# Optimization experiments

Measured on AMD Instinct MI355X. Metric: run time of the kernel, lower is better.

The kernel has to match this reference:

```python
import jax, jax.numpy as jnp
import numpy as np

B, S, D, H = 4, 2048, 512, 8
DH = D // H


def setup_inputs() -> dict:
    key = jax.random.key(0)
    ks = jax.random.split(key, 7)
    scale = 1.0 / np.sqrt(DH)  # mimic nn.Linear init magnitude
    return {
        "x": jax.random.normal(ks[0], (B, S, D), dtype=jnp.float32),
        "Wq": jax.random.normal(ks[1], (H, DH, DH), dtype=jnp.float32) * scale,
        "bq": jax.random.normal(ks[2], (H, DH), dtype=jnp.float32) * scale,
        "Wk": jax.random.normal(ks[3], (H, DH, DH), dtype=jnp.float32) * scale,
        "bk": jax.random.normal(ks[4], (H, DH), dtype=jnp.float32) * scale,
        "Wv": jax.random.normal(ks[5], (H, DH, DH), dtype=jnp.float32) * scale,
        "bv": jax.random.normal(ks[6], (H, DH), dtype=jnp.float32) * scale,
    }


def reference(x, Wq, bq, Wk, bk, Wv, bv):
    # x: [B, S, D] -> per-head slices [B, S, H, DH] (contiguous chunks, as in torch slicing)
    xh = x.reshape(B, S, H, DH)
    # nn.Linear: y = x @ W.T + b, per head. Wq[h] is [out, in].
    q = jnp.einsum("bshd,hed->bshe", xh, Wq) + bq  # [B, S, H, DH]
    k = jnp.einsum("bshd,hed->bshe", xh, Wk) + bk
    v = jnp.einsum("bshd,hed->bshe", xh, Wv) + bv
    scores = jnp.einsum("bshe,bthe->bhst", q, k) / jnp.sqrt(jnp.float32(DH))  # [B, H, S, S]
    attn = jax.nn.softmax(scores, axis=-1)
    out = jnp.einsum("bhst,bthe->bshe", attn, v)  # [B, S, H, DH]
    return out.reshape(B, S, D)  # hstack of head outputs == concat along feature dim
```

## Files before the change

kernel.cpp:

```cpp
#include <hip/hip_runtime.h>
#include <math.h>

#define B_ 4
#define S_ 2048
#define D_ 512
#define H_ 8
#define DH_ 64
#define BH_ (B_*H_)
#define SCALE 0.1803368801111243f

typedef __attribute__((ext_vector_type(4)))  float f32x4;
typedef __attribute__((ext_vector_type(16))) float f32x16;
typedef __attribute__((ext_vector_type(8)))  short bf16x8;
typedef __attribute__((ext_vector_type(4)))  uint  u32x4;

__device__ inline uint rnepk(float a, float b) {
    uint ua = __builtin_bit_cast(uint, a), ub = __builtin_bit_cast(uint, b);
    ua += 0x7FFFu + ((ua >> 16) & 1u);
    ub += 0x7FFFu + ((ub >> 16) & 1u);
    return (ua >> 16) | (ub & 0xFFFF0000u);
}
__device__ inline uint truncpk(float lo, float hi) {
    return __builtin_amdgcn_perm(__builtin_bit_cast(uint, hi),
                                 __builtin_bit_cast(uint, lo), 0x07060302u);
}
__device__ inline f32x16 zero16() {
    f32x16 z;
    #pragma unroll
    for (int i = 0; i < 16; ++i) z[i] = 0.f;
    return z;
}
__device__ inline bf16x8 pack8(f32x4 a, f32x4 c) {
    u32x4 u;
    u.x = rnepk(a[0], a[1]); u.y = rnepk(a[2], a[3]);
    u.z = rnepk(c[0], c[1]); u.w = rnepk(c[2], c[3]);
    return __builtin_bit_cast(bf16x8, u);
}

#if __has_builtin(__builtin_amdgcn_permlane32_swap)
__device__ inline void lane32swap(uint& a, uint& b) {
    typedef __attribute__((ext_vector_type(2))) uint u32x2;
    u32x2 r = __builtin_amdgcn_permlane32_swap(a, b, false, false);
    a = r.x; b = r.y;
}
#else
__device__ inline void lane32swap(uint& a, uint& b) {
    const int l5 = (threadIdx.x & 63) >> 5;
    uint send = l5 ? a : b;
    uint recv = __shfl_xor(send, 32);
    uint an = l5 ? recv : a;
    uint bn = l5 ? b : recv;
    a = an; b = bn;
}
#endif

__device__ inline void dma16(const ushort* g, ushort* l) {
    __builtin_amdgcn_global_load_lds(
        (const __attribute__((address_space(1))) unsigned int*)g,
        (__attribute__((address_space(3))) unsigned int*)l, 16, 0, 0);
}

__global__ __launch_bounds__(256)
void prep_w(const float* __restrict__ Wq, const float* __restrict__ Wk,
            const float* __restrict__ Wv, ushort* __restrict__ Wf)
{
    const int pb = blockIdx.x;
    const int proj = pb >> 3, h = pb & 7;
    const float* W = (proj == 0 ? Wq : proj == 1 ? Wk : Wv) + h * DH_ * DH_;
    #pragma unroll
    for (int it = 0; it < 2; ++it) {
        const int slot = threadIdx.x + it * 256;
        const int c = slot >> 6, lane = slot & 63;
        const int l31 = lane & 31, l5 = lane >> 5;
        const int et = c >> 2, st = c & 3;
        const float* wr = W + (et * 32 + l31) * DH_ + st * 16 + l5 * 8;
        bf16x8 v = pack8(*(const f32x4*)wr, *(const f32x4*)(wr + 4));
        *(bf16x8*)(Wf + ((size_t)pb * 8 + c) * 512 + lane * 8) = v;
    }
}

__global__ __launch_bounds__(256, 2)
void qkv_mfma(const float* __restrict__ x,
              const float* __restrict__ bq, const float* __restrict__ bk,
              const float* __restrict__ bv, const ushort* __restrict__ Wf,
              ushort* __restrict__ Qf, ushort* __restrict__ Kf,
              ushort* __restrict__ Vf)
{
    const int bh = blockIdx.x, b = bh >> 3, h = bh & 7;
    const int sblk = blockIdx.y, s0 = sblk * 128;
    const int tid = threadIdx.x;
    const int w = tid >> 6, lane = tid & 63, l31 = lane & 31, l5 = lane >> 5;

    __shared__ __align__(16) ushort bnc[4][2560];
    __shared__ __align__(16) ushort vsh[64 * 136];
    ushort* mybnc = bnc[w];

    const ushort* wqb = Wf + ((size_t)(0 * 8 + h)) * 8 * 512;
    const ushort* wkb = Wf + ((size_t)(1 * 8 + h)) * 8 * 512;
    const ushort* wvb = Wf + ((size_t)(2 * 8 + h)) * 8 * 512;

    const int srow = w * 32 + l31;
    const float* xr = x + ((size_t)(b * S_ + s0 + srow)) * D_ + h * DH_;
    bf16x8 xf[4];
    #pragma unroll
    for (int st = 0; st < 4; ++st)
        xf[st] = pack8(*(const f32x4*)(xr + st * 16 + l5 * 8),
                       *(const f32x4*)(xr + st * 16 + l5 * 8 + 4));

    {
        bf16x8 wf[2][4];
        #pragma unroll
        for (int et = 0; et < 2; ++et)
            #pragma unroll
            for (int st = 0; st < 4; ++st)
                wf[et][st] = *(const bf16x8*)(wkb + (et * 4 + st) * 512 + lane * 8);
        #pragma unroll
        for (int et = 0; et < 2; ++et) {
            f32x16 acc = zero16();
            #pragma unroll
            for (int st = 0; st < 4; ++st)
                acc = __builtin_amdgcn_mfma_f32_32x32x16_bf16(wf[et][st], xf[st], acc, 0, 0, 0);
            #pragma unroll
            for (int rg = 0; rg < 4; ++rg) {
                float4 b4 = *(const float4*)(bk + h * DH_ + et * 32 + rg * 8 + l5 * 4);
                uint2 pk;
                pk.x = rnepk(acc[rg * 4 + 0] + b4.x, acc[rg * 4 + 1] + b4.y);
                pk.y = rnepk(acc[rg * 4 + 2] + b4.z, acc[rg * 4 + 3] + b4.w);
                *(uint2*)(mybnc + l31 * 72 + et * 32 + rg * 8 + l5 * 4) = pk;
            }
        }
        const int kt = sblk * 2 + (w >> 1), g = w & 1;
        ushort* kd = Kf + (((size_t)(bh * 32 + kt)) * 2 + g) * 2048;
        #pragma unroll
        for (int st = 0; st < 4; ++st) {
            uint4 v = *(const uint4*)(mybnc + l31 * 72 + st * 16 + l5 * 8);
            *(uint4*)(kd + st * 512 + lane * 8) = v;
        }
    }

    {
        bf16x8 wf[2][4];
        #pragma unroll
        for (int et = 0; et < 2; ++et)
            #pragma unroll
            for (int st = 0; st < 4; ++st)
                wf[et][st] = *(const bf16x8*)(wqb + (et * 4 + st) * 512 + lane * 8);
        #pragma unroll
        for (int et = 0; et < 2; ++et) {
            f32x16 acc = zero16();
            #pragma unroll
            for (int st = 0; st < 4; ++st)
                acc = __builtin_amdgcn_mfma_f32_32x32x16_bf16(wf[et][st], xf[st], acc, 0, 0, 0);
            #pragma unroll
            for (int rg = 0; rg < 4; ++rg) {
                float4 b4 = *(const float4*)(bq + h * DH_ + et * 32 + rg * 8 + l5 * 4);
                uint2 pk;
                pk.x = rnepk((acc[rg * 4 + 0] + b4.x) * SCALE, (acc[rg * 4 + 1] + b4.y) * SCALE);
                pk.y = rnepk((acc[rg * 4 + 2] + b4.z) * SCALE, (acc[rg * 4 + 3] + b4.w) * SCALE);
                *(uint2*)(mybnc + l31 * 72 + et * 32 + rg * 8 + l5 * 4) = pk;
            }
        }
        ushort* qd = Qf + ((size_t)(bh * 64 + sblk * 4 + w)) * 2048;
        #pragma unroll
        for (int st = 0; st < 4; ++st) {
            uint4 v = *(const uint4*)(mybnc + l31 * 72 + st * 16 + l5 * 8);
            *(uint4*)(qd + st * 512 + lane * 8) = v;
        }
    }

    {
        bf16x8 wf[2][4];
        #pragma unroll
        for (int et = 0; et < 2; ++et)
            #pragma unroll
            for (int st = 0; st < 4; ++st)
                wf[et][st] = *(const bf16x8*)(wvb + (et * 4 + st) * 512 + lane * 8);
        #pragma unroll
        for (int et = 0; et < 2; ++et) {
            f32x16 acc = zero16();
            #pragma unroll
            for (int st = 0; st < 4; ++st)
                acc = __builtin_amdgcn_mfma_f32_32x32x16_bf16(xf[st], wf[et][st], acc, 0, 0, 0);
            const float bb = bv[h * DH_ + et * 32 + l31];
            #pragma unroll
            for (int rg = 0; rg < 4; ++rg) {
                uint2 pk;
                pk.x = rnepk(acc[rg * 4 + 0] + bb, acc[rg * 4 + 1] + bb);
                pk.y = rnepk(acc[rg * 4 + 2] + bb, acc[rg * 4 + 3] + bb);
                *(uint2*)(vsh + (et * 32 + l31) * 136 + w * 32 + rg * 8 + l5 * 4) = pk;
            }
        }
        __syncthreads();
        #pragma unroll
        for (int i = 0; i < 4; ++i) {
            const int c = w * 4 + i;
            const int ktl = c >> 3, dht = (c >> 2) & 1, st = c & 3;
            uint4 v = *(const uint4*)(vsh + (dht * 32 + l31) * 136 + ktl * 64 + st * 16 + l5 * 8);
            *(uint4*)(Vf + (((size_t)(bh * 32 + sblk * 2 + ktl)) * 2 + dht) * 2048
                      + st * 512 + lane * 8) = v;
        }
    }
}

__global__ __launch_bounds__(256, 2)
void flash_mfma(const ushort* __restrict__ Qf, const ushort* __restrict__ Kf,
                const ushort* __restrict__ Vf, float* __restrict__ out)
{
    const int blk = blockIdx.x;
    const int bh = blk & 31, qblk = blk >> 5;
    const int b = bh >> 3, h = bh & 7;
    const int tid = threadIdx.x;
    const int w = tid >> 6, lane = tid & 63, l31 = lane & 31, l5 = lane >> 5;
    const int p = w >> 1, qh = w & 1;

    __shared__ __align__(16) ushort lds_u[32768];

    const ushort* kvsrc = (w & 1) ? (Vf + (size_t)bh * 32 * 4096)
                                  : (Kf + (size_t)bh * 32 * 4096);

    {
        const ushort* gb = kvsrc + (size_t)p * 4096;
        ushort* ld = lds_u + w * 4096;
        #pragma unroll
        for (int i = 0; i < 8; ++i)
            dma16(gb + i * 512 + lane * 8, ld + i * 512);
    }

    bf16x8 qf[2][4];
    #pragma unroll
    for (int qt = 0; qt < 2; ++qt)
        #pragma unroll
        for (int st = 0; st < 4; ++st)
            qf[qt][st] = *(const bf16x8*)(Qf + ((size_t)(bh * 64 + qblk * 4 + qh * 2 + qt)) * 2048
                                          + st * 512 + lane * 8);

    f32x16 O[2][2];
    #pragma unroll
    for (int i = 0; i < 2; ++i)
        #pragma unroll
        for (int j = 0; j < 2; ++j) O[i][j] = zero16();
    float lsum[2] = {0.f, 0.f};

    for (int step = 0; step < 16; ++step) {
        __syncthreads();
        ushort* cbuf = lds_u + (step & 1) * 16384;
        if (step < 15) {
            const ushort* gb = kvsrc + (size_t)(2 * (step + 1) + p) * 4096;
            ushort* ld = lds_u + ((step + 1) & 1) * 16384 + w * 4096;
            #pragma unroll
            for (int i = 0; i < 8; ++i)
                dma16(gb + i * 512 + lane * 8, ld + i * 512);
        }
        const ushort* kreg = cbuf + p * 8192;
        const ushort* vreg = kreg + 4096;

        bf16x8 pf[2][4];
        #pragma unroll
        for (int g = 0; g < 2; ++g) {
            bf16x8 kf[4];
            #pragma unroll
            for (int st = 0; st < 4; ++st)
                kf[st] = *(const bf16x8*)(kreg + (g * 4 + st) * 512 + lane * 8);
            #pragma unroll
            for (int qt = 0; qt < 2; ++qt) {
                f32x16 sc_ = zero16();
                __builtin_amdgcn_s_setprio(1);
                #pragma unroll
                for (int st = 0; st < 4; ++st)
                    sc_ = __builtin_amdgcn_mfma_f32_32x32x16_bf16(kf[st], qf[qt][st], sc_, 0, 0, 0);
                __builtin_amdgcn_s_setprio(0);
                uint pr[8];
                #pragma unroll
                for (int rg = 0; rg < 4; ++rg) {
                    float p0 = __builtin_amdgcn_exp2f(sc_[rg * 4 + 0]);
                    float p1 = __builtin_amdgcn_exp2f(sc_[rg * 4 + 1]);
                    float p2 = __builtin_amdgcn_exp2f(sc_[rg * 4 + 2]);
                    float p3 = __builtin_amdgcn_exp2f(sc_[rg * 4 + 3]);
                    lsum[qt] += (p0 + p1) + (p2 + p3);
                    pr[2 * rg + 0] = truncpk(p0, p1);
                    pr[2 * rg + 1] = truncpk(p2, p3);
                }
                #pragma unroll
                for (int pp = 0; pp < 2; ++pp) {
                    lane32swap(pr[4 * pp + 0], pr[4 * pp + 2]);
                    lane32swap(pr[4 * pp + 1], pr[4 * pp + 3]);
                    u32x4 u; u.x = pr[4 * pp + 0]; u.y = pr[4 * pp + 1];
                    u.z = pr[4 * pp + 2]; u.w = pr[4 * pp + 3];
                    pf[qt][g * 2 + pp] = __builtin_bit_cast(bf16x8, u);
                }
            }
        }

        #pragma unroll
        for (int dht = 0; dht < 2; ++dht) {
            bf16x8 vf[4];
            #pragma unroll
            for (int st = 0; st < 4; ++st)
                vf[st] = *(const bf16x8*)(vreg + (dht * 4 + st) * 512 + lane * 8);
            __builtin_amdgcn_s_setprio(1);
            #pragma unroll
            for (int qt = 0; qt < 2; ++qt)
                #pragma unroll
                for (int st = 0; st < 4; ++st)
                    O[dht][qt] = __builtin_amdgcn_mfma_f32_32x32x16_bf16(vf[st], pf[qt][st],
                                                                          O[dht][qt], 0, 0, 0);
            __builtin_amdgcn_s_setprio(0);
        }
    }

    #pragma unroll
    for (int qt = 0; qt < 2; ++qt) lsum[qt] += __shfl_xor(lsum[qt], 32);

    __syncthreads();
    float* mb = (float*)lds_u;
    float* reg = mb + qh * 4352;
    float* lsA = mb + 2 * 4352;

    if (p == 1) {
        #pragma unroll
        for (int dht = 0; dht < 2; ++dht)
            #pragma unroll
            for (int qt = 0; qt < 2; ++qt)
                #pragma unroll
                for (int rg = 0; rg < 4; ++rg) {
                    f32x4 v4;
                    v4[0] = O[dht][qt][rg * 4 + 0];
                    v4[1] = O[dht][qt][rg * 4 + 1];
                    v4[2] = O[dht][qt][rg * 4 + 2];
                    v4[3] = O[dht][qt][rg * 4 + 3];
                    *(f32x4*)(reg + (qt * 32 + l31) * 68 + dht * 32 + rg * 8 + l5 * 4) = v4;
                }
        if (l5 == 0) {
            #pragma unroll
            for (int qt = 0; qt < 2; ++qt)
                lsA[qh * 64 + qt * 32 + l31] = lsum[qt];
        }
    }
    __syncthreads();
    if (p == 0) {
        float linv[2];
        #pragma unroll
        for (int qt = 0; qt < 2; ++qt)
            linv[qt] = 1.0f / (lsum[qt] + lsA[qh * 64 + qt * 32 + l31]);
        #pragma unroll
        for (int dht = 0; dht < 2; ++dht)
            #pragma unroll
            for (int qt = 0; qt < 2; ++qt)
                #pragma unroll
                for (int rg = 0; rg < 4; ++rg) {
                    float* a = reg + (qt * 32 + l31) * 68 + dht * 32 + rg * 8 + l5 * 4;
                    f32x4 part = *(const f32x4*)a;
                    f32x4 v4;
                    v4[0] = (O[dht][qt][rg * 4 + 0] + part[0]) * linv[qt];
                    v4[1] = (O[dht][qt][rg * 4 + 1] + part[1]) * linv[qt];
                    v4[2] = (O[dht][qt][rg * 4 + 2] + part[2]) * linv[qt];
                    v4[3] = (O[dht][qt][rg * 4 + 3] + part[3]) * linv[qt];
                    *(f32x4*)a = v4;
                }
    }
    __syncthreads();

    const int q0 = qblk * 128;
    #pragma unroll
    for (int i = 0; i < 8; ++i) {
        const int slot = tid + 256 * i;
        const int r = slot >> 4, c = slot & 15;
        f32x4 v = *(const f32x4*)(mb + (r >> 6) * 4352 + (r & 63) * 68 + c * 4);
        *(f32x4*)(out + ((size_t)(b * S_ + q0 + r)) * D_ + h * DH_ + c * 4) = v;
    }
}

extern "C" void kernel_launch(void* const* d_in, const int* in_sizes, int n_in,
                              void* d_out, int out_size, void* d_ws, size_t ws_size,
                              hipStream_t stream) {
    const float* x  = (const float*)d_in[0];
    const float* Wq = (const float*)d_in[1];
    const float* bq = (const float*)d_in[2];
    const float* Wk = (const float*)d_in[3];
    const float* bk = (const float*)d_in[4];
    const float* Wv = (const float*)d_in[5];
    const float* bv = (const float*)d_in[6];
    float* outp = (float*)d_out;

    ushort* Qf = (ushort*)d_ws;
    ushort* Kf = Qf + (size_t)BH_ * S_ * DH_;
    ushort* Vf = Kf + (size_t)BH_ * S_ * DH_;
    ushort* Wfb = Vf + (size_t)BH_ * S_ * DH_;

    prep_w<<<dim3(24), 256, 0, stream>>>(Wq, Wk, Wv, Wfb);
    qkv_mfma<<<dim3(BH_, S_ / 128), 256, 0, stream>>>(x, bq, bk, bv, Wfb,
                                                      Qf, Kf, Vf);
    flash_mfma<<<dim3(32 * 16), 256, 0, stream>>>(Qf, Kf, Vf, outp);
}
```

Baseline: 125.2 us.

## Drop LDS staging of K/V in attention, load tiles directly from global

The attention kernel no longer double-buffers K/V tiles into LDS with async global-to-LDS copies. Each wave now reads its K and V fragments straight from global/L2. The query block per workgroup is halved to 64 rows with one Q tile per wave, and the grid doubles to 32x32 blocks with launch bounds raised to 4 blocks per CU. This removes per-step barriers and LDS traffic and is meant to raise occupancy, at the cost of redundant global K/V reads across more blocks and the loss of load latency hiding.

Result: slower. 129.9 us (+3.7%).

```diff
diff --git a/kernel.cpp b/kernel.cpp
--- a/kernel.cpp
+++ b/kernel.cpp
@@ -53,12 +53,6 @@
     a = an; b = bn;
 }
 #endif
-
-__device__ inline void dma16(const ushort* g, ushort* l) {
-    __builtin_amdgcn_global_load_lds(
-        (const __attribute__((address_space(1))) unsigned int*)g,
-        (__attribute__((address_space(3))) unsigned int*)l, 16, 0, 0);
-}
 
 __global__ __launch_bounds__(256)
 void prep_w(const float* __restrict__ Wq, const float* __restrict__ Wk,
@@ -202,92 +196,67 @@
     }
 }
 
-__global__ __launch_bounds__(256, 2)
+__global__ __launch_bounds__(256, 4)
 void flash_mfma(const ushort* __restrict__ Qf, const ushort* __restrict__ Kf,
                 const ushort* __restrict__ Vf, float* __restrict__ out)
 {
-    const int blk = blockIdx.x;
-    const int bh = blk & 31, qblk = blk >> 5;
+    const int bh = blockIdx.x, qblk2 = blockIdx.y;
     const int b = bh >> 3, h = bh & 7;
     const int tid = threadIdx.x;
     const int w = tid >> 6, lane = tid & 63, l31 = lane & 31, l5 = lane >> 5;
-    const int p = w >> 1, qh = w & 1;
-
-    __shared__ __align__(16) ushort lds_u[32768];
-
-    const ushort* kvsrc = (w & 1) ? (Vf + (size_t)bh * 32 * 4096)
-                                  : (Kf + (size_t)bh * 32 * 4096);
-
-    {
-        const ushort* gb = kvsrc + (size_t)p * 4096;
-        ushort* ld = lds_u + w * 4096;
-        #pragma unroll
-        for (int i = 0; i < 8; ++i)
-            dma16(gb + i * 512 + lane * 8, ld + i * 512);
-    }
-
-    bf16x8 qf[2][4];
-    #pragma unroll
-    for (int qt = 0; qt < 2; ++qt)
-        #pragma unroll
-        for (int st = 0; st < 4; ++st)
-            qf[qt][st] = *(const bf16x8*)(Qf + ((size_t)(bh * 64 + qblk * 4 + qh * 2 + qt)) * 2048
-                                          + st * 512 + lane * 8);
-
-    f32x16 O[2][2];
-    #pragma unroll
-    for (int i = 0; i < 2; ++i)
-        #pragma unroll
-        for (int j = 0; j < 2; ++j) O[i][j] = zero16();
-    float lsum[2] = {0.f, 0.f};
+    const int qh = w >> 1, p = w & 1;
+
+    __shared__ __align__(16) float mb[2 * 32 * 68 + 64];
+
+    const ushort* kbase = Kf + (size_t)bh * 32 * 4096;
+    const ushort* vbase = Vf + (size_t)bh * 32 * 4096;
+
+    bf16x8 qf[4];
+    #pragma unroll
+    for (int st = 0; st < 4; ++st)
+        qf[st] = *(const bf16x8*)(Qf + ((size_t)(bh * 64 + qblk2 * 2 + qh)) * 2048
+                                  + st * 512 + lane * 8);
+
+    f32x16 O[2];
+    O[0] = zero16(); O[1] = zero16();
+    float lsum = 0.f;
 
     for (int step = 0; step < 16; ++step) {
-        __syncthreads();
-        ushort* cbuf = lds_u + (step & 1) * 16384;
-        if (step < 15) {
-            const ushort* gb = kvsrc + (size_t)(2 * (step + 1) + p) * 4096;
-            ushort* ld = lds_u + ((step + 1) & 1) * 16384 + w * 4096;
-            #pragma unroll
-            for (int i = 0; i < 8; ++i)
-                dma16(gb + i * 512 + lane * 8, ld + i * 512);
-        }
-        const ushort* kreg = cbuf + p * 8192;
-        const ushort* vreg = kreg + 4096;
-
-        bf16x8 pf[2][4];
+        const int kt = 2 * step + p;
+        const ushort* ktile = kbase + (size_t)kt * 4096;
+        const ushort* vtile = vbase + (size_t)kt * 4096;
+
+        bf16x8 pf[4];
         #pragma unroll
         for (int g = 0; g < 2; ++g) {
             bf16x8 kf[4];
             #pragma unroll
             for (int st = 0; st < 4; ++st)
-                kf[st] = *(const bf16x8*)(kreg + (g * 4 + st) * 512 + lane * 8);
-            #pragma unroll
-            for (int qt = 0; qt < 2; ++qt) {
-                f32x16 sc_ = zero16();
-                __builtin_amdgcn_s_setprio(1);
-                #pragma unroll
-                for (int st = 0; st < 4; ++st)
-                    sc_ = __builtin_amdgcn_mfma_f32_32x32x16_bf16(kf[st], qf[qt][st], sc_, 0, 0, 0);
-                __builtin_amdgcn_s_setprio(0);
-                uint pr[8];
-                #pragma unroll
-                for (int rg = 0; rg < 4; ++rg) {
-                    float p0 = __builtin_amdgcn_exp2f(sc_[rg * 4 + 0]);
-                    float p1 = __builtin_amdgcn_exp2f(sc_[rg * 4 + 1]);
-                    float p2 = __builtin_amdgcn_exp2f(sc_[rg * 4 + 2]);
-                    float p3 = __builtin_amdgcn_exp2f(sc_[rg * 4 + 3]);
-                    lsum[qt] += (p0 + p1) + (p2 + p3);
-                    pr[2 * rg + 0] = truncpk(p0, p1);
-                    pr[2 * rg + 1] = truncpk(p2, p3);
-                }
-                #pragma unroll
-                for (int pp = 0; pp < 2; ++pp) {
-                    lane32swap(pr[4 * pp + 0], pr[4 * pp + 2]);
-                    lane32swap(pr[4 * pp + 1], pr[4 * pp + 3]);
-                    u32x4 u; u.x = pr[4 * pp + 0]; u.y = pr[4 * pp + 1];
-                    u.z = pr[4 * pp + 2]; u.w = pr[4 * pp + 3];
-                    pf[qt][g * 2 + pp] = __builtin_bit_cast(bf16x8, u);
-                }
+                kf[st] = *(const bf16x8*)(ktile + (g * 4 + st) * 512 + lane * 8);
+            f32x16 sc_ = zero16();
+            __builtin_amdgcn_s_setprio(1);
+            #pragma unroll
+            for (int st = 0; st < 4; ++st)
+                sc_ = __builtin_amdgcn_mfma_f32_32x32x16_bf16(kf[st], qf[st], sc_, 0, 0, 0);
+            __builtin_amdgcn_s_setprio(0);
+            uint pr[8];
+            #pragma unroll
+            for (int rg = 0; rg < 4; ++rg) {
+                float p0 = __builtin_amdgcn_exp2f(sc_[rg * 4 + 0]);
+                float p1 = __builtin_amdgcn_exp2f(sc_[rg * 4 + 1]);
+                float p2 = __builtin_amdgcn_exp2f(sc_[rg * 4 + 2]);
+                float p3 = __builtin_amdgcn_exp2f(sc_[rg * 4 + 3]);
+                lsum += (p0 + p1) + (p2 + p3);
+                pr[2 * rg + 0] = truncpk(p0, p1);
+                pr[2 * rg + 1] = truncpk(p2, p3);
+            }
+            #pragma unroll
+            for (int pp = 0; pp < 2; ++pp) {
+                lane32swap(pr[4 * pp + 0], pr[4 * pp + 2]);
+                lane32swap(pr[4 * pp + 1], pr[4 * pp + 3]);
+                u32x4 u; u.x = pr[4 * pp + 0]; u.y = pr[4 * pp + 1];
+                u.z = pr[4 * pp + 2]; u.w = pr[4 * pp + 3];
+                pf[g * 2 + pp] = __builtin_bit_cast(bf16x8, u);
             }
         }
 
@@ -296,76 +265,59 @@
             bf16x8 vf[4];
             #pragma unroll
             for (int st = 0; st < 4; ++st)
-                vf[st] = *(const bf16x8*)(vreg + (dht * 4 + st) * 512 + lane * 8);
+                vf[st] = *(const bf16x8*)(vtile + (dht * 4 + st) * 512 + lane * 8);
             __builtin_amdgcn_s_setprio(1);
             #pragma unroll
-            for (int qt = 0; qt < 2; ++qt)
-                #pragma unroll
-                for (int st = 0; st < 4; ++st)
-                    O[dht][qt] = __builtin_amdgcn_mfma_f32_32x32x16_bf16(vf[st], pf[qt][st],
-                                                                          O[dht][qt], 0, 0, 0);
+            for (int st = 0; st < 4; ++st)
+                O[dht] = __builtin_amdgcn_mfma_f32_32x32x16_bf16(vf[st], pf[st], O[dht], 0, 0, 0);
             __builtin_amdgcn_s_setprio(0);
         }
     }
 
-    #pragma unroll
-    for (int qt = 0; qt < 2; ++qt) lsum[qt] += __shfl_xor(lsum[qt], 32);
-
-    __syncthreads();
-    float* mb = (float*)lds_u;
-    float* reg = mb + qh * 4352;
-    float* lsA = mb + 2 * 4352;
+    lsum += __shfl_xor(lsum, 32);
+
+    float* reg = mb + qh * 2176;
+    float* lsA = mb + 2 * 2176;
 
     if (p == 1) {
         #pragma unroll
         for (int dht = 0; dht < 2; ++dht)
             #pragma unroll
-            for (int qt = 0; qt < 2; ++qt)
-                #pragma unroll
-                for (int rg = 0; rg < 4; ++rg) {
-                    f32x4 v4;
-                    v4[0] = O[dht][qt][rg * 4 + 0];
-                    v4[1] = O[dht][qt][rg * 4 + 1];
-                    v4[2] = O[dht][qt][rg * 4 + 2];
-                    v4[3] = O[dht][qt][rg * 4 + 3];
-                    *(f32x4*)(reg + (qt * 32 + l31) * 68 + dht * 32 + rg * 8 + l5 * 4) = v4;
-                }
-        if (l5 == 0) {
-            #pragma unroll
-            for (int qt = 0; qt < 2; ++qt)
-                lsA[qh * 64 + qt * 32 + l31] = lsum[qt];
-        }
+            for (int rg = 0; rg < 4; ++rg) {
+                f32x4 v4;
+                v4[0] = O[dht][rg * 4 + 0];
+                v4[1] = O[dht][rg * 4 + 1];
+                v4[2] = O[dht][rg * 4 + 2];
+                v4[3] = O[dht][rg * 4 + 3];
+                *(f32x4*)(reg + l31 * 68 + dht * 32 + rg * 8 + l5 * 4) = v4;
+            }
+        if (l5 == 0) lsA[qh * 32 + l31] = lsum;
     }
     __syncthreads();
     if (p == 0) {
-        float linv[2];
-        #pragma unroll
-        for (int qt = 0; qt < 2; ++qt)
-            linv[qt] = 1.0f / (lsum[qt] + lsA[qh * 64 + qt * 32 + l31]);
+        const float linv = 1.0f / (lsum + lsA[qh * 32 + l31]);
         #pragma unroll
         for (int dht = 0; dht < 2; ++dht)
             #pragma unroll
-            for (int qt = 0; qt < 2; ++qt)
-                #pragma unroll
-                for (int rg = 0; rg < 4; ++rg) {
-                    float* a = reg + (qt * 32 + l31) * 68 + dht * 32 + rg * 8 + l5 * 4;
-                    f32x4 part = *(const f32x4*)a;
-                    f32x4 v4;
-                    v4[0] = (O[dht][qt][rg * 4 + 0] + part[0]) * linv[qt];
-                    v4[1] = (O[dht][qt][rg * 4 + 1] + part[1]) * linv[qt];
-                    v4[2] = (O[dht][qt][rg * 4 + 2] + part[2]) * linv[qt];
-                    v4[3] = (O[dht][qt][rg * 4 + 3] + part[3]) * linv[qt];
-                    *(f32x4*)a = v4;
-                }
+            for (int rg = 0; rg < 4; ++rg) {
+                float* a = reg + l31 * 68 + dht * 32 + rg * 8 + l5 * 4;
+                f32x4 part = *(const f32x4*)a;
+                f32x4 v4;
+                v4[0] = (O[dht][rg * 4 + 0] + part[0]) * linv;
+                v4[1] = (O[dht][rg * 4 + 1] + part[1]) * linv;
+                v4[2] = (O[dht][rg * 4 + 2] + part[2]) * linv;
+                v4[3] = (O[dht][rg * 4 + 3] + part[3]) * linv;
+                *(f32x4*)a = v4;
+            }
     }
     __syncthreads();
 
-    const int q0 = qblk * 128;
-    #pragma unroll
-    for (int i = 0; i < 8; ++i) {
+    const int q0 = qblk2 * 64;
+    #pragma unroll
+    for (int i = 0; i < 4; ++i) {
         const int slot = tid + 256 * i;
         const int r = slot >> 4, c = slot & 15;
-        f32x4 v = *(const f32x4*)(mb + (r >> 6) * 4352 + (r & 63) * 68 + c * 4);
+        f32x4 v = *(const f32x4*)(mb + (r >> 5) * 2176 + (r & 31) * 68 + c * 4);
         *(f32x4*)(out + ((size_t)(b * S_ + q0 + r)) * D_ + h * DH_ + c * 4) = v;
     }
 }
@@ -382,13 +334,13 @@
     const float* bv = (const float*)d_in[6];
     float* outp = (float*)d_out;
 
-    ushort* Qf = (ushort*)d_ws;
-    ushort* Kf = Qf + (size_t)BH_ * S_ * DH_;
-    ushort* Vf = Kf + (size_t)BH_ * S_ * DH_;
+    ushort* Qf  = (ushort*)d_ws;
+    ushort* Kf  = Qf + (size_t)BH_ * S_ * DH_;
+    ushort* Vf  = Kf + (size_t)BH_ * S_ * DH_;
     ushort* Wfb = Vf + (size_t)BH_ * S_ * DH_;
 
     prep_w<<<dim3(24), 256, 0, stream>>>(Wq, Wk, Wv, Wfb);
     qkv_mfma<<<dim3(BH_, S_ / 128), 256, 0, stream>>>(x, bq, bk, bv, Wfb,
                                                       Qf, Kf, Vf);
-    flash_mfma<<<dim3(32 * 16), 256, 0, stream>>>(Qf, Kf, Vf, outp);
-}
+    flash_mfma<<<dim3(BH_, 32), 256, 0, stream>>>(Qf, Kf, Vf, outp);
+}
```
